# Performance work log

Hardware: AMD Instinct MI355X
Metric: run time of the kernel (lower is better)

## Reference

```python
import jax, jax.numpy as jnp
import numpy as np

N = 50000
SELF_LOOP_W = 2.0  # GCNConv(improved=True)


def gcn_conv(x, edge_index, W, b):
    # x: [N, Fin], edge_index: [2, E] (row=source, col=target)
    h = x @ W  # [N, Fout]
    row, col = edge_index[0], edge_index[1]
    ones = jnp.ones(row.shape[0], dtype=h.dtype)
    deg = jax.ops.segment_sum(ones, col, num_segments=N) + SELF_LOOP_W
    dinv = jnp.where(deg > 0, jax.lax.rsqrt(deg), 0.0)
    norm = dinv[row] * dinv[col]  # [E]
    agg = jax.ops.segment_sum(norm[:, None] * h[row], col, num_segments=N)
    # self-loop contribution: weight 2.0, norm = dinv[i]^2
    agg = agg + (SELF_LOOP_W * dinv * dinv)[:, None] * h
    return agg + b


def setup_inputs() -> dict:
    key = jax.random.key(0)
    ks = jax.random.split(key, 12)
    F_in, H1, H2, H3 = 256, 256, 128, 64
    E, Ep, En = 800000, 200000, 200000
    def glorot(k, shape):
        lim = np.sqrt(6.0 / (shape[0] + shape[1]))
        return jax.random.uniform(k, shape, jnp.float32, -lim, lim)
    return {
        "x": jax.random.normal(ks[0], (N, F_in), jnp.float32),
        "train_edge_index": jax.random.randint(ks[1], (2, E), 0, N),
        "pos_edge_index": jax.random.randint(ks[2], (2, Ep), 0, N),
        "neg_edge_index": jax.random.randint(ks[3], (2, En), 0, N),
        "W1": glorot(ks[4], (F_in, H1)),
        "b1": jnp.zeros((H1,), jnp.float32),
        "W2": glorot(ks[5], (H1, H2)),
        "b2": jnp.zeros((H2,), jnp.float32),
        "Wl1": glorot(ks[6], (H2, H3)),
        "bl1": jnp.zeros((H3,), jnp.float32),
        "Wl2": glorot(ks[7], (H3, 1)),
        "bl2": jnp.zeros((1,), jnp.float32),
    }


def reference(x, train_edge_index, pos_edge_index, neg_edge_index,
              W1, b1, W2, b2, Wl1, bl1, Wl2, bl2):
    h = jax.nn.relu(gcn_conv(x, train_edge_index, W1, b1))
    h = gcn_conv(h, train_edge_index, W2, b2)  # [N, 128]
    tei = jnp.concatenate([pos_edge_index, neg_edge_index], axis=-1)  # [2, Ep+En]
    e = h[tei[1]] + h[tei[0]]  # x_i + x_j, [Etot, 128]
    e = jax.nn.relu(e @ Wl1 + bl1)
    e = jax.nn.sigmoid(e @ Wl2 + bl2)
    return e.reshape(-1)
```

## Files before the change

kernel.cpp:

```cpp
#include <hip/hip_runtime.h>
#include <math.h>

#define NV 50000
#define ETR 800000
#define EPOS 200000
#define ETEST 400000

typedef __attribute__((ext_vector_type(8))) short bf16x8;
typedef __attribute__((ext_vector_type(8))) unsigned short ushortx8;
typedef __attribute__((ext_vector_type(4))) float f32x4;

__device__ inline unsigned short f2b(float f) {
    union { float f; unsigned u; } v; v.f = f;
    unsigned r = v.u + 0x7fffu + ((v.u >> 16) & 1u);
    return (unsigned short)(r >> 16);
}
__device__ inline float blo(unsigned q) { union { unsigned u; float f; } v; v.u = q << 16; return v.f; }
__device__ inline float bhi(unsigned q) { union { unsigned u; float f; } v; v.u = q & 0xffff0000u; return v.f; }
__device__ inline float b2f(unsigned short s) { union { unsigned u; float f; } v; v.u = ((unsigned)s) << 16; return v.f; }

__device__ inline ushortx8 bf16add8(ushortx8 a, ushortx8 b) {
    ushortx8 r;
    #pragma unroll
    for (int i = 0; i < 8; ++i)
        r[i] = f2b(b2f(a[i]) + b2f(b[i]));
    return r;
}


__global__ void deg_kernel(const int* __restrict__ tei, int* __restrict__ deg) {
    int e = blockIdx.x * blockDim.x + threadIdx.x;
    if (e < ETR) atomicAdd(&deg[tei[ETR + e]], 1);
}

__global__ __launch_bounds__(1024) void partial_kernel(const int* __restrict__ deg,
                                                       int* __restrict__ partials) {
    int i = blockIdx.x * 1024 + threadIdx.x;
    int v = (i < NV) ? deg[i] : 0;
    #pragma unroll
    for (int off = 32; off > 0; off >>= 1) v += __shfl_xor(v, off);
    __shared__ int wsum[16];
    if ((threadIdx.x & 63) == 0) wsum[threadIdx.x >> 6] = v;
    __syncthreads();
    if (threadIdx.x == 0) {
        int s = 0;
        #pragma unroll
        for (int k = 0; k < 16; ++k) s += wsum[k];
        partials[blockIdx.x] = s;
    }
}

__global__ __launch_bounds__(1024) void ptr_kernel(
    const int* __restrict__ deg, const int* __restrict__ partials,
    int* __restrict__ ptr, int* __restrict__ cursor, float* __restrict__ dinv)
{
    int b = blockIdx.x, t = threadIdx.x;
    int i = b * 1024 + t;
    int d = (i < NV) ? deg[i] : 0;
    int lane = t & 63, w = t >> 6;
    int v = d;
    #pragma unroll
    for (int off = 1; off < 64; off <<= 1) {
        int u = __shfl_up(v, off);
        if (lane >= off) v += u;
    }
    __shared__ int wsum[16], woff[16];
    if (lane == 63) wsum[w] = v;
    __syncthreads();
    if (t == 0) {
        int s = 0;
        for (int k = 0; k < b; ++k) s += partials[k];
        for (int k = 0; k < 16; ++k) { woff[k] = s; s += wsum[k]; }
    }
    __syncthreads();
    int excl = woff[w] + v - d;
    if (i < NV) {
        ptr[i] = excl;
        cursor[i] = excl;
        dinv[i] = rsqrtf((float)d + 2.0f);
        if (i == NV - 1) ptr[NV] = excl + d;
    }
}

__global__ void fill_kernel(const int* __restrict__ tei, const float* __restrict__ dinv,
                            int* __restrict__ cursor, int2* __restrict__ edat) {
    int e = blockIdx.x * blockDim.x + threadIdx.x;
    if (e < ETR) {
        int row = tei[e];
        int col = tei[ETR + e];
        int p = atomicAdd(&cursor[col], 1);
        edat[p] = make_int2(row, __float_as_int(dinv[row] * dinv[col]));
    }
}


__global__ void cvt_x_kernel(const float* __restrict__ x, unsigned short* __restrict__ xb, int n4) {
    int i = blockIdx.x * blockDim.x + threadIdx.x;
    if (i < n4) {
        float4 v = *(const float4*)&x[i * 4];
        union { unsigned short u[4]; uint2 q; } o;
        o.u[0] = f2b(v.x); o.u[1] = f2b(v.y); o.u[2] = f2b(v.z); o.u[3] = f2b(v.w);
        *(uint2*)&xb[i * 4] = o.q;
    }
}

__global__ void cvt_wt_kernel(const float* __restrict__ W, unsigned short* __restrict__ Wt,
                              int K, int N) {
    int idx = blockIdx.x * blockDim.x + threadIdx.x;
    if (idx < N * K) {
        int n = idx / K, k = idx - n * K;
        Wt[idx] = f2b(W[k * N + n]);
    }
}


template<int N, int K>
__global__ __launch_bounds__(256) void mfma_gemm_kernel(
    const unsigned short* __restrict__ A, const unsigned short* __restrict__ Bt,
    unsigned short* __restrict__ C, int M)
{
    constexpr int BK = 64;
    __shared__ unsigned short Asm[128][BK];
    __shared__ unsigned short Bsm[128][BK];
    int tid = threadIdx.x;
    int lane = tid & 63, wid = tid >> 6;
    int wr = wid >> 1, wc = wid & 1;
    int row0 = blockIdx.x * 128, col0 = blockIdx.y * 128;

    int sr = tid >> 3;
    int s8 = tid & 7;
    int sswz = s8 ^ (sr & 7);
    int fr = lane & 15;
    int g  = lane >> 4;

    f32x4 acc[4][4] = {};

    for (int k0 = 0; k0 < K; k0 += BK) {
        #pragma unroll
        for (int i = 0; i < 4; ++i) {
            int r = sr + i * 32;
            int gr = row0 + r;
            ushortx8 va = {0, 0, 0, 0, 0, 0, 0, 0};
            if (gr < M) va = *(const ushortx8*)&A[(size_t)gr * K + k0 + s8 * 8];
            *(ushortx8*)&Asm[r][sswz * 8] = va;
            ushortx8 vb = *(const ushortx8*)&Bt[(size_t)(col0 + r) * K + k0 + s8 * 8];
            *(ushortx8*)&Bsm[r][sswz * 8] = vb;
        }
        __syncthreads();
        #pragma unroll
        for (int kf = 0; kf < BK; kf += 32) {
            int sbase = kf >> 3;
            bf16x8 af[4], bfr[4];
            #pragma unroll
            for (int m = 0; m < 4; ++m) {
                int rr = wr * 64 + m * 16 + fr;
                af[m] = *(const bf16x8*)&Asm[rr][((sbase + g) ^ (fr & 7)) * 8];
            }
            #pragma unroll
            for (int n = 0; n < 4; ++n) {
                int rr = wc * 64 + n * 16 + fr;
                bfr[n] = *(const bf16x8*)&Bsm[rr][((sbase + g) ^ (fr & 7)) * 8];
            }
            #pragma unroll
            for (int m = 0; m < 4; ++m)
                #pragma unroll
                for (int n = 0; n < 4; ++n)
                    acc[m][n] = __builtin_amdgcn_mfma_f32_16x16x32_bf16(af[m], bfr[n], acc[m][n], 0, 0, 0);
        }
        __syncthreads();
    }

    #pragma unroll
    for (int m = 0; m < 4; ++m) {
        int rbase = row0 + wr * 64 + m * 16 + g * 4;
        #pragma unroll
        for (int j = 0; j < 4; ++j) {
            int r = rbase + j;
            if (r < M) {
                #pragma unroll
                for (int n = 0; n < 4; ++n) {
                    int c = col0 + wc * 64 + n * 16 + fr;
                    C[(size_t)r * N + c] = f2b(acc[m][n][j]);
                }
            }
        }
    }
}


template<int F, bool RELU>
__global__ __launch_bounds__(256) void gather_kernel(
    const int* __restrict__ ptr, const int2* __restrict__ edat,
    const float* __restrict__ dinv, const unsigned short* __restrict__ hlin,
    const float* __restrict__ bias, unsigned short* __restrict__ hout)
{
    constexpr int V = F / 64;
    int gid = blockIdx.x * blockDim.x + threadIdx.x;
    int node = gid >> 6, lane = gid & 63;
    if (node >= NV) return;
    float dc = dinv[node];
    int j0 = ptr[node], j1 = ptr[node + 1];
    float acc[V] = {};
    const unsigned short* hb = hlin + lane * V;

    int j = j0;
    for (; j + 3 < j1; j += 4) {
        int2 e0 = edat[j],     e1 = edat[j + 1];
        int2 e2 = edat[j + 2], e3 = edat[j + 3];
        float n0 = __int_as_float(e0.y), n1 = __int_as_float(e1.y);
        float n2 = __int_as_float(e2.y), n3 = __int_as_float(e3.y);
        if constexpr (V == 4) {
            uint2 q0 = *(const uint2*)(hb + (size_t)e0.x * F);
            uint2 q1 = *(const uint2*)(hb + (size_t)e1.x * F);
            uint2 q2 = *(const uint2*)(hb + (size_t)e2.x * F);
            uint2 q3 = *(const uint2*)(hb + (size_t)e3.x * F);
            acc[0] += n0 * blo(q0.x) + n1 * blo(q1.x) + n2 * blo(q2.x) + n3 * blo(q3.x);
            acc[1] += n0 * bhi(q0.x) + n1 * bhi(q1.x) + n2 * bhi(q2.x) + n3 * bhi(q3.x);
            acc[2] += n0 * blo(q0.y) + n1 * blo(q1.y) + n2 * blo(q2.y) + n3 * blo(q3.y);
            acc[3] += n0 * bhi(q0.y) + n1 * bhi(q1.y) + n2 * bhi(q2.y) + n3 * bhi(q3.y);
        } else {
            unsigned q0 = *(const unsigned*)(hb + (size_t)e0.x * F);
            unsigned q1 = *(const unsigned*)(hb + (size_t)e1.x * F);
            unsigned q2 = *(const unsigned*)(hb + (size_t)e2.x * F);
            unsigned q3 = *(const unsigned*)(hb + (size_t)e3.x * F);
            acc[0] += n0 * blo(q0) + n1 * blo(q1) + n2 * blo(q2) + n3 * blo(q3);
            acc[1] += n0 * bhi(q0) + n1 * bhi(q1) + n2 * bhi(q2) + n3 * bhi(q3);
        }
    }
    for (; j < j1; ++j) {
        int2 e0 = edat[j];
        float n0 = __int_as_float(e0.y);
        if constexpr (V == 4) {
            uint2 q0 = *(const uint2*)(hb + (size_t)e0.x * F);
            acc[0] += n0 * blo(q0.x);
            acc[1] += n0 * bhi(q0.x);
            acc[2] += n0 * blo(q0.y);
            acc[3] += n0 * bhi(q0.y);
        } else {
            unsigned q0 = *(const unsigned*)(hb + (size_t)e0.x * F);
            acc[0] += n0 * blo(q0);
            acc[1] += n0 * bhi(q0);
        }
    }

    const unsigned short* ps = hb + (size_t)node * F;
    float sw = 2.0f * dc * dc;
    if constexpr (V == 4) {
        uint2 qs = *(const uint2*)ps;
        float o0 = acc[0] + sw * blo(qs.x) + bias[lane * 4 + 0];
        float o1 = acc[1] + sw * bhi(qs.x) + bias[lane * 4 + 1];
        float o2 = acc[2] + sw * blo(qs.y) + bias[lane * 4 + 2];
        float o3 = acc[3] + sw * bhi(qs.y) + bias[lane * 4 + 3];
        if (RELU) {
            o0 = fmaxf(o0, 0.f); o1 = fmaxf(o1, 0.f);
            o2 = fmaxf(o2, 0.f); o3 = fmaxf(o3, 0.f);
        }
        union { unsigned short u[4]; unsigned long long ll; } pk;
        pk.u[0] = f2b(o0); pk.u[1] = f2b(o1); pk.u[2] = f2b(o2); pk.u[3] = f2b(o3);
        __builtin_nontemporal_store(pk.ll, (unsigned long long*)(hout + (size_t)node * F + lane * 4));
    } else {
        unsigned qs = *(const unsigned*)ps;
        float o0 = acc[0] + sw * blo(qs) + bias[lane * 2 + 0];
        float o1 = acc[1] + sw * bhi(qs) + bias[lane * 2 + 1];
        if (RELU) { o0 = fmaxf(o0, 0.f); o1 = fmaxf(o1, 0.f); }
        union { unsigned short u[2]; unsigned q; } pk;
        pk.u[0] = f2b(o0); pk.u[1] = f2b(o1);
        __builtin_nontemporal_store(pk.q, (unsigned*)(hout + (size_t)node * F + lane * 2));
    }
}


__global__ __launch_bounds__(256) void edge_mlp_mfma_kernel(
    const int* __restrict__ pos, const int* __restrict__ neg,
    const unsigned short* __restrict__ h2, const unsigned short* __restrict__ Wl1t,
    const float* __restrict__ bl1, const float* __restrict__ Wl2,
    const float* __restrict__ bl2, float* __restrict__ out)
{
    __shared__ unsigned short Es[128][128];
    __shared__ unsigned short Ws[64][128];
    int tid = threadIdx.x;
    int lane = tid & 63, w = tid >> 6;
    int fr = lane & 15, g = lane >> 4;
    int e0 = blockIdx.x * 128;

    #pragma unroll
    for (int k = 0; k < 4; ++k) {
        int chunk = tid + k * 256;
        int row = chunk >> 4, c = chunk & 15;
        *(ushortx8*)&Ws[row][(c ^ (row & 7)) * 8] = *(const ushortx8*)&Wl1t[chunk * 8];
    }

    int et = tid >> 1, hh = tid & 1;
    int eg = e0 + et;
    int a, b;
    if (eg < EPOS) { a = pos[eg]; b = pos[EPOS + eg]; }
    else { int i = eg - EPOS; a = neg[i]; b = neg[EPOS + i]; }
    const unsigned short* pa = h2 + (size_t)a * 128 + hh * 64;
    const unsigned short* pb = h2 + (size_t)b * 128 + hh * 64;
    #pragma unroll
    for (int c8 = 0; c8 < 8; ++c8) {
        ushortx8 va = *(const ushortx8*)&pa[c8 * 8];
        ushortx8 vb = *(const ushortx8*)&pb[c8 * 8];
        ushortx8 vs = bf16add8(va, vb);
        int c = hh * 8 + c8;
        *(ushortx8*)&Es[et][(c ^ (et & 7)) * 8] = vs;
    }
    __syncthreads();

    f32x4 acc[2][4] = {};
    #pragma unroll
    for (int ks = 0; ks < 4; ++ks) {
        int c = ks * 4 + g;
        bf16x8 af[2], bfr[4];
        #pragma unroll
        for (int m = 0; m < 2; ++m) {
            int r = w * 32 + m * 16 + fr;
            af[m] = *(const bf16x8*)&Es[r][(c ^ (r & 7)) * 8];
        }
        #pragma unroll
        for (int n = 0; n < 4; ++n) {
            int r = n * 16 + fr;
            bfr[n] = *(const bf16x8*)&Ws[r][(c ^ (r & 7)) * 8];
        }
        #pragma unroll
        for (int m = 0; m < 2; ++m)
            #pragma unroll
            for (int n = 0; n < 4; ++n)
                acc[m][n] = __builtin_amdgcn_mfma_f32_16x16x32_bf16(af[m], bfr[n], acc[m][n], 0, 0, 0);
    }

    float bl2v = bl2[0];
    float b1v[4], w2v[4];
    #pragma unroll
    for (int n = 0; n < 4; ++n) {
        b1v[n] = bl1[n * 16 + fr];
        w2v[n] = Wl2[n * 16 + fr];
    }
    #pragma unroll
    for (int m = 0; m < 2; ++m) {
        float p[4];
        #pragma unroll
        for (int j = 0; j < 4; ++j) {
            float s = 0.f;
            #pragma unroll
            for (int n = 0; n < 4; ++n)
                s += fmaxf(acc[m][n][j] + b1v[n], 0.0f) * w2v[n];
            p[j] = s;
        }
        #pragma unroll
        for (int off = 1; off < 16; off <<= 1) {
            #pragma unroll
            for (int j = 0; j < 4; ++j)
                p[j] += __shfl_xor(p[j], off);
        }
        int ebase = e0 + w * 32 + m * 16 + g * 4;
        #pragma unroll
        for (int j = 0; j < 4; ++j)
            if (fr == j)
                out[ebase + j] = 1.0f / (1.0f + expf(-(p[j] + bl2v)));
    }
}


extern "C" void kernel_launch(void* const* d_in, const int* in_sizes, int n_in,
                              void* d_out, int out_size, void* d_ws, size_t ws_size,
                              hipStream_t stream) {
    const float* x   = (const float*)d_in[0];
    const int*   tei = (const int*)d_in[1];
    const int*   pos = (const int*)d_in[2];
    const int*   neg = (const int*)d_in[3];
    const float* W1  = (const float*)d_in[4];
    const float* b1  = (const float*)d_in[5];
    const float* W2  = (const float*)d_in[6];
    const float* b2  = (const float*)d_in[7];
    const float* Wl1 = (const float*)d_in[8];
    const float* bl1 = (const float*)d_in[9];
    const float* Wl2 = (const float*)d_in[10];
    const float* bl2 = (const float*)d_in[11];
    float* out = (float*)d_out;

    float* fws = (float*)d_ws;
    int*   iws = (int*)d_ws;
    unsigned short* usws = (unsigned short*)d_ws;
    float* dinv     = fws;
    int*   deg      = iws + 50000;
    int*   ptr      = iws + 100000;
    int*   cursor   = iws + 150002;
    int2*  edat     = (int2*)(iws + 200064);
    int*   partials = iws + 1800064;
    unsigned short* w1t  = usws + 2ull * 1800192;
    unsigned short* w2t  = usws + 2ull * 1832960;
    unsigned short* wl1t = usws + 2ull * 1849344;
    unsigned short* bufX = usws + 2ull * 1853504;
    unsigned short* bufL16 = usws + 2ull * 8253504;
    unsigned short* bufH = usws + 2ull * 14653504;

    hipMemsetAsync(deg, 0, NV * sizeof(int), stream);

    deg_kernel<<<(ETR + 255) / 256, 256, 0, stream>>>(tei, deg);
    partial_kernel<<<49, 1024, 0, stream>>>(deg, partials);
    ptr_kernel<<<49, 1024, 0, stream>>>(deg, partials, ptr, cursor, dinv);
    fill_kernel<<<(ETR + 255) / 256, 256, 0, stream>>>(tei, dinv, cursor, edat);

    cvt_x_kernel<<<(NV * 256 / 4 + 255) / 256, 256, 0, stream>>>(x, bufX, NV * 256 / 4);
    cvt_wt_kernel<<<(256 * 256 + 255) / 256, 256, 0, stream>>>(W1, w1t, 256, 256);
    cvt_wt_kernel<<<(128 * 256 + 255) / 256, 256, 0, stream>>>(W2, w2t, 256, 128);
    cvt_wt_kernel<<<(64 * 128 + 255) / 256, 256, 0, stream>>>(Wl1, wl1t, 128, 64);

    mfma_gemm_kernel<256, 256><<<dim3(391, 2), 256, 0, stream>>>(bufX, w1t, bufL16, NV);
    gather_kernel<256, true><<<(NV * 64) / 256, 256, 0, stream>>>(ptr, edat, dinv, bufL16, b1, bufH);

    mfma_gemm_kernel<128, 256><<<dim3(391, 1), 256, 0, stream>>>(bufH, w2t, bufX, NV);
    gather_kernel<128, false><<<(NV * 64) / 256, 256, 0, stream>>>(ptr, edat, dinv, bufX, b2, bufL16);

    edge_mlp_mfma_kernel<<<ETEST / 128, 256, 0, stream>>>(pos, neg, bufL16, wl1t, bl1, Wl2, bl2, out);
}
```

Baseline: 300.1 us.

## Fuse fp32-to-bf16 input conversion into GEMM, merge weight casts, deepen gather unroll

Removes the standalone x conversion kernel and instead converts fp32 x to bf16 while loading A tiles in the first GEMM. This drops a full write and re-read of the bf16 copy of x. The three weight transpose-and-cast kernels are merged into one launch. The gather kernel now unrolls by 8 with nontemporal edge-list loads to keep more independent loads in flight. The cost is that the first GEMM reads twice as many bytes for A, and the deeper unroll raises register pressure.

```diff
diff --git a/kernel.cpp b/kernel.cpp
--- a/kernel.cpp
+++ b/kernel.cpp
@@ -94,29 +94,29 @@
 }
 
 
-__global__ void cvt_x_kernel(const float* __restrict__ x, unsigned short* __restrict__ xb, int n4) {
-    int i = blockIdx.x * blockDim.x + threadIdx.x;
-    if (i < n4) {
-        float4 v = *(const float4*)&x[i * 4];
-        union { unsigned short u[4]; uint2 q; } o;
-        o.u[0] = f2b(v.x); o.u[1] = f2b(v.y); o.u[2] = f2b(v.z); o.u[3] = f2b(v.w);
-        *(uint2*)&xb[i * 4] = o.q;
-    }
-}
-
-__global__ void cvt_wt_kernel(const float* __restrict__ W, unsigned short* __restrict__ Wt,
-                              int K, int N) {
+__global__ void cvt_wt_all_kernel(const float* __restrict__ W1, const float* __restrict__ W2,
+                                  const float* __restrict__ Wl1,
+                                  unsigned short* __restrict__ w1t, unsigned short* __restrict__ w2t,
+                                  unsigned short* __restrict__ wl1t) {
     int idx = blockIdx.x * blockDim.x + threadIdx.x;
-    if (idx < N * K) {
-        int n = idx / K, k = idx - n * K;
-        Wt[idx] = f2b(W[k * N + n]);
-    }
-}
-
-
-template<int N, int K>
+    if (idx < 65536) {
+        int n = idx >> 8, k = idx & 255;
+        w1t[idx] = f2b(W1[k * 256 + n]);
+    } else if (idx < 98304) {
+        int i = idx - 65536;
+        int n = i >> 8, k = i & 255;
+        w2t[i] = f2b(W2[k * 128 + n]);
+    } else if (idx < 106496) {
+        int i = idx - 98304;
+        int n = i >> 7, k = i & 127;
+        wl1t[i] = f2b(Wl1[k * 64 + n]);
+    }
+}
+
+
+template<int N, int K, bool AF32>
 __global__ __launch_bounds__(256) void mfma_gemm_kernel(
-    const unsigned short* __restrict__ A, const unsigned short* __restrict__ Bt,
+    const void* __restrict__ Av, const unsigned short* __restrict__ Bt,
     unsigned short* __restrict__ C, int M)
 {
     constexpr int BK = 64;
@@ -141,7 +141,18 @@
             int r = sr + i * 32;
             int gr = row0 + r;
             ushortx8 va = {0, 0, 0, 0, 0, 0, 0, 0};
-            if (gr < M) va = *(const ushortx8*)&A[(size_t)gr * K + k0 + s8 * 8];
+            if constexpr (AF32) {
+                const float* Af = (const float*)Av;
+                if (gr < M) {
+                    float4 f0 = *(const float4*)&Af[(size_t)gr * K + k0 + s8 * 8];
+                    float4 f1 = *(const float4*)&Af[(size_t)gr * K + k0 + s8 * 8 + 4];
+                    va[0] = f2b(f0.x); va[1] = f2b(f0.y); va[2] = f2b(f0.z); va[3] = f2b(f0.w);
+                    va[4] = f2b(f1.x); va[5] = f2b(f1.y); va[6] = f2b(f1.z); va[7] = f2b(f1.w);
+                }
+            } else {
+                const unsigned short* Ab = (const unsigned short*)Av;
+                if (gr < M) va = *(const ushortx8*)&Ab[(size_t)gr * K + k0 + s8 * 8];
+            }
             *(ushortx8*)&Asm[r][sswz * 8] = va;
             ushortx8 vb = *(const ushortx8*)&Bt[(size_t)(col0 + r) * K + k0 + s8 * 8];
             *(ushortx8*)&Bsm[r][sswz * 8] = vb;
@@ -202,42 +213,80 @@
     int j0 = ptr[node], j1 = ptr[node + 1];
     float acc[V] = {};
     const unsigned short* hb = hlin + lane * V;
+    const long long* edl = (const long long*)edat;
 
     int j = j0;
+    for (; j + 7 < j1; j += 8) {
+        long long e[8];
+        #pragma unroll
+        for (int u = 0; u < 8; ++u) e[u] = __builtin_nontemporal_load(edl + j + u);
+        if constexpr (V == 4) {
+            uint2 q[8];
+            #pragma unroll
+            for (int u = 0; u < 8; ++u)
+                q[u] = *(const uint2*)(hb + (size_t)(int)e[u] * F);
+            #pragma unroll
+            for (int u = 0; u < 8; ++u) {
+                float n = __int_as_float((int)(e[u] >> 32));
+                acc[0] += n * blo(q[u].x);
+                acc[1] += n * bhi(q[u].x);
+                acc[2] += n * blo(q[u].y);
+                acc[3] += n * bhi(q[u].y);
+            }
+        } else {
+            unsigned q[8];
+            #pragma unroll
+            for (int u = 0; u < 8; ++u)
+                q[u] = *(const unsigned*)(hb + (size_t)(int)e[u] * F);
+            #pragma unroll
+            for (int u = 0; u < 8; ++u) {
+                float n = __int_as_float((int)(e[u] >> 32));
+                acc[0] += n * blo(q[u]);
+                acc[1] += n * bhi(q[u]);
+            }
+        }
+    }
     for (; j + 3 < j1; j += 4) {
-        int2 e0 = edat[j],     e1 = edat[j + 1];
-        int2 e2 = edat[j + 2], e3 = edat[j + 3];
-        float n0 = __int_as_float(e0.y), n1 = __int_as_float(e1.y);
-        float n2 = __int_as_float(e2.y), n3 = __int_as_float(e3.y);
+        long long e[4];
+        #pragma unroll
+        for (int u = 0; u < 4; ++u) e[u] = __builtin_nontemporal_load(edl + j + u);
         if constexpr (V == 4) {
-            uint2 q0 = *(const uint2*)(hb + (size_t)e0.x * F);
-            uint2 q1 = *(const uint2*)(hb + (size_t)e1.x * F);
-            uint2 q2 = *(const uint2*)(hb + (size_t)e2.x * F);
-            uint2 q3 = *(const uint2*)(hb + (size_t)e3.x * F);
-            acc[0] += n0 * blo(q0.x) + n1 * blo(q1.x) + n2 * blo(q2.x) + n3 * blo(q3.x);
-            acc[1] += n0 * bhi(q0.x) + n1 * bhi(q1.x) + n2 * bhi(q2.x) + n3 * bhi(q3.x);
-            acc[2] += n0 * blo(q0.y) + n1 * blo(q1.y) + n2 * blo(q2.y) + n3 * blo(q3.y);
-            acc[3] += n0 * bhi(q0.y) + n1 * bhi(q1.y) + n2 * bhi(q2.y) + n3 * bhi(q3.y);
+            uint2 q[4];
+            #pragma unroll
+            for (int u = 0; u < 4; ++u)
+                q[u] = *(const uint2*)(hb + (size_t)(int)e[u] * F);
+            #pragma unroll
+            for (int u = 0; u < 4; ++u) {
+                float n = __int_as_float((int)(e[u] >> 32));
+                acc[0] += n * blo(q[u].x);
+                acc[1] += n * bhi(q[u].x);
+                acc[2] += n * blo(q[u].y);
+                acc[3] += n * bhi(q[u].y);
+            }
         } else {
-            unsigned q0 = *(const unsigned*)(hb + (size_t)e0.x * F);
-            unsigned q1 = *(const unsigned*)(hb + (size_t)e1.x * F);
-            unsigned q2 = *(const unsigned*)(hb + (size_t)e2.x * F);
-            unsigned q3 = *(const unsigned*)(hb + (size_t)e3.x * F);
-            acc[0] += n0 * blo(q0) + n1 * blo(q1) + n2 * blo(q2) + n3 * blo(q3);
-            acc[1] += n0 * bhi(q0) + n1 * bhi(q1) + n2 * bhi(q2) + n3 * bhi(q3);
+            unsigned q[4];
+            #pragma unroll
+            for (int u = 0; u < 4; ++u)
+                q[u] = *(const unsigned*)(hb + (size_t)(int)e[u] * F);
+            #pragma unroll
+            for (int u = 0; u < 4; ++u) {
+                float n = __int_as_float((int)(e[u] >> 32));
+                acc[0] += n * blo(q[u]);
+                acc[1] += n * bhi(q[u]);
+            }
         }
     }
     for (; j < j1; ++j) {
-        int2 e0 = edat[j];
-        float n0 = __int_as_float(e0.y);
+        long long e0 = __builtin_nontemporal_load(edl + j);
+        float n0 = __int_as_float((int)(e0 >> 32));
         if constexpr (V == 4) {
-            uint2 q0 = *(const uint2*)(hb + (size_t)e0.x * F);
+            uint2 q0 = *(const uint2*)(hb + (size_t)(int)e0 * F);
             acc[0] += n0 * blo(q0.x);
             acc[1] += n0 * bhi(q0.x);
             acc[2] += n0 * blo(q0.y);
             acc[3] += n0 * bhi(q0.y);
         } else {
-            unsigned q0 = *(const unsigned*)(hb + (size_t)e0.x * F);
+            unsigned q0 = *(const unsigned*)(hb + (size_t)(int)e0 * F);
             acc[0] += n0 * blo(q0);
             acc[1] += n0 * bhi(q0);
         }
@@ -401,16 +450,12 @@
     partial_kernel<<<49, 1024, 0, stream>>>(deg, partials);
     ptr_kernel<<<49, 1024, 0, stream>>>(deg, partials, ptr, cursor, dinv);
     fill_kernel<<<(ETR + 255) / 256, 256, 0, stream>>>(tei, dinv, cursor, edat);
-
-    cvt_x_kernel<<<(NV * 256 / 4 + 255) / 256, 256, 0, stream>>>(x, bufX, NV * 256 / 4);
-    cvt_wt_kernel<<<(256 * 256 + 255) / 256, 256, 0, stream>>>(W1, w1t, 256, 256);
-    cvt_wt_kernel<<<(128 * 256 + 255) / 256, 256, 0, stream>>>(W2, w2t, 256, 128);
-    cvt_wt_kernel<<<(64 * 128 + 255) / 256, 256, 0, stream>>>(Wl1, wl1t, 128, 64);
-
-    mfma_gemm_kernel<256, 256><<<dim3(391, 2), 256, 0, stream>>>(bufX, w1t, bufL16, NV);
+    cvt_wt_all_kernel<<<416, 256, 0, stream>>>(W1, W2, Wl1, w1t, w2t, wl1t);
+
+    mfma_gemm_kernel<256, 256, true><<<dim3(391, 2), 256, 0, stream>>>(x, w1t, bufL16, NV);
     gather_kernel<256, true><<<(NV * 64) / 256, 256, 0, stream>>>(ptr, edat, dinv, bufL16, b1, bufH);
 
-    mfma_gemm_kernel<128, 256><<<dim3(391, 1), 256, 0, stream>>>(bufH, w2t, bufX, NV);
+    mfma_gemm_kernel<128, 256, false><<<dim3(391, 1), 256, 0, stream>>>(bufH, w2t, bufX, NV);
     gather_kernel<128, false><<<(NV * 64) / 256, 256, 0, stream>>>(ptr, edat, dinv, bufX, b2, bufL16);
 
     edge_mlp_mfma_kernel<<<ETEST / 128, 256, 0, stream>>>(pos, neg, bufL16, wl1t, bl1, Wl2, bl2, out);
```

Result: no change. 298.1 us (-0.7%).
